# Performance work log

Hardware: AMD Instinct MI355X
Metric: run time of the kernel (lower is better)

Reference implementation:

```python
import jax, jax.numpy as jnp
import numpy as np
from jax import lax

DN = ('NCHW', 'OIHW', 'NCHW')
BN_EPS = 1e-5


def _conv(x, w, pad):
    # pad: list of (lo, hi) for H, W
    return lax.conv_general_dilated(x, w, (1, 1), pad, dimension_numbers=DN)


def _grid_sample_bilinear(img, grid):
    """F.grid_sample(img, grid, align_corners=True, padding_mode='zeros').
    img: [N,C,H,W], grid: [N,Ho,Wo,2] with (x,y) in [-1,1]."""
    N, C, H, W = img.shape
    gx, gy = grid[..., 0], grid[..., 1]
    # align_corners=True mapping to pixel coords
    ix = (gx + 1.0) * 0.5 * (W - 1)
    iy = (gy + 1.0) * 0.5 * (H - 1)
    x0 = jnp.floor(ix)
    y0 = jnp.floor(iy)
    x1 = x0 + 1.0
    y1 = y0 + 1.0
    # bilinear weights
    wa = (x1 - ix) * (y1 - iy)  # top-left (x0,y0)
    wb = (ix - x0) * (y1 - iy)  # top-right (x1,y0)
    wc = (x1 - ix) * (iy - y0)  # bottom-left (x0,y1)
    wd = (ix - x0) * (iy - y0)  # bottom-right (x1,y1)

    imgc = jnp.transpose(img, (0, 2, 3, 1))  # [N,H,W,C]
    b = jnp.arange(N)[:, None, None]

    def gather(xi, yi):
        valid = (xi >= 0) & (xi <= W - 1) & (yi >= 0) & (yi <= H - 1)
        xc = jnp.clip(xi, 0, W - 1).astype(jnp.int32)
        yc = jnp.clip(yi, 0, H - 1).astype(jnp.int32)
        v = imgc[b, yc, xc]  # [N,Ho,Wo,C]
        return v * valid[..., None].astype(img.dtype)

    out = (gather(x0, y0) * wa[..., None] + gather(x1, y0) * wb[..., None]
           + gather(x0, y1) * wc[..., None] + gather(x1, y1) * wd[..., None])
    return jnp.transpose(out, (0, 3, 1, 2))  # [N,C,Ho,Wo]


def setup_inputs() -> dict:
    key = jax.random.key(0)
    ks = jax.random.split(key, 12)
    N, C1, C2 = 8, 512, 256
    H, W = 64, 64
    x1 = jax.random.normal(ks[0], (N, C1, 2 * H, 2 * W), dtype=jnp.float32)
    x2 = jax.random.normal(ks[1], (N, C2, H, W), dtype=jnp.float32)
    w_change = jax.random.normal(ks[2], (C2, C1, 1, 1), dtype=jnp.float32) * 0.02
    b_change = jax.random.normal(ks[3], (C2,), dtype=jnp.float32) * 0.02
    w_cc1 = jax.random.normal(ks[4], (C2, 2 * C2, 1, 1), dtype=jnp.float32) * 0.02
    bn_gamma = 1.0 + 0.1 * jax.random.normal(ks[5], (C2,), dtype=jnp.float32)
    bn_beta = 0.1 * jax.random.normal(ks[6], (C2,), dtype=jnp.float32)
    bn_mean = 0.1 * jax.random.normal(ks[7], (C2,), dtype=jnp.float32)
    bn_var = jax.random.uniform(ks[8], (C2,), dtype=jnp.float32, minval=0.5, maxval=1.5)
    w_cc2 = jax.random.normal(ks[9], (4, C2, 3, 3), dtype=jnp.float32) * 0.02
    return {"x1": x1, "x2": x2, "w_change": w_change, "b_change": b_change,
            "w_cc1": w_cc1, "bn_gamma": bn_gamma, "bn_beta": bn_beta,
            "bn_mean": bn_mean, "bn_var": bn_var, "w_cc2": w_cc2}


def reference(x1, x2, w_change, b_change, w_cc1, bn_gamma, bn_beta, bn_mean, bn_var, w_cc2):
    # MaxPool2d(2,2)
    x1p = lax.reduce_window(x1, -jnp.inf, lax.max, (1, 1, 2, 2), (1, 1, 2, 2), 'VALID')
    # change: 1x1 conv with bias
    x1c = _conv(x1p, w_change, [(0, 0), (0, 0)]) + b_change[None, :, None, None]
    # concat + concat_conv (1x1 conv -> BN(eval) -> ReLU -> 3x3 conv)
    x = jnp.concatenate([x1c, x2], axis=1)
    x = _conv(x, w_cc1, [(0, 0), (0, 0)])
    inv = lax.rsqrt(bn_var + BN_EPS)
    x = (x - bn_mean[None, :, None, None]) * (inv * bn_gamma)[None, :, None, None] + bn_beta[None, :, None, None]
    x = jax.nn.relu(x)
    flow = _conv(x, w_cc2, [(1, 1), (1, 1)])  # [N,4,H,W]
    flow1 = flow[:, :2]
    flow2 = flow[:, 2:]

    N, _, H, W = x1c.shape
    # base grid: [...,0]=x over width, [...,1]=y over height
    xs = jnp.linspace(-1.0, 1.0, W, dtype=x1c.dtype)
    ys = jnp.linspace(-1.0, 1.0, H, dtype=x1c.dtype)
    base = jnp.stack(jnp.meshgrid(xs, ys, indexing='xy'), axis=-1)  # [H,W,2]
    norm = jnp.array([(W - 1) / 2.0, (H - 1) / 2.0], dtype=x1c.dtype)

    grid1 = base[None] + jnp.transpose(flow1, (0, 2, 3, 1)) / norm
    grid2 = base[None] + jnp.transpose(flow2, (0, 2, 3, 1)) / norm

    u1 = _grid_sample_bilinear(x1c, grid1)
    u2 = _grid_sample_bilinear(x2, grid2)
    return u1 + u2
```

## Files before the change

### kernel.cpp

```cpp
#include <hip/hip_runtime.h>
#include <hip/hip_bf16.h>

#define NB 8
#define C1 512
#define C2 256
#define HWSZ 4096
#define BN_EPS 1e-5f
#define P2 264

typedef __hip_bfloat16 bf16;
typedef __hip_bfloat162 bf162;
typedef __attribute__((ext_vector_type(8))) short short8v;
typedef __attribute__((ext_vector_type(4))) float f32x4;

static __device__ inline float us2f(unsigned short u) {
  union { unsigned u32; float f; } c; c.u32 = ((unsigned)u) << 16; return c.f;
}

static __device__ inline unsigned short f2bf(float f) {
  union { bf16 h; unsigned short u; } c;
  c.h = __float2bfloat16(f);
  return c.u;
}

static __device__ inline uint2 pack4(float a, float b, float c, float d) {
  union { uint2 u; bf162 h[2]; } pk;
  pk.h[0] = __float22bfloat162_rn(make_float2(a, b));
  pk.h[1] = __float22bfloat162_rn(make_float2(c, d));
  return pk.u;
}

#define SWA(m_, c_)  (((((c_) >> 3) ^ (((m_) >> 3) & 3)) << 3) + ((c_) & 7))
#define SWA2(m_, c_) (((((c_) >> 3) ^ (((m_) >> 3) & 7)) << 3) + ((c_) & 7))

#define SBARQ() asm volatile("s_waitcnt lgkmcnt(0)\n\ts_barrier" ::: "memory")
#define SBAR()  asm volatile("s_barrier" ::: "memory")
#define LGKM0() asm volatile("s_waitcnt lgkmcnt(0)" ::: "memory")

__global__ __launch_bounds__(256) void k0_prep(
    const float* __restrict__ wch, const float* __restrict__ wcc1,
    const float* __restrict__ wcc2,
    unsigned short* __restrict__ wchB, unsigned short* __restrict__ wcc1B,
    float* __restrict__ wr, float* __restrict__ flow) {
  const int t = blockIdx.x * 256 + threadIdx.x;
  if (t < 262144) {
    const int which = t >> 17;
    const int r = t & 131071;
    const int i = r & 7;
    const int lane = (r >> 3) & 63;
    const int ntile = (r >> 9) & 15;
    const int kstep = r >> 13;
    const int ci = kstep * 32 + (lane >> 4) * 8 + i;
    const int co = ntile * 16 + (lane & 15);
    const float* s = which ? wcc1 : wch;
    unsigned short* d = which ? wcc1B : wchB;
    d[r] = f2bf(s[co * 512 + ci]);
  } else if (t < 262144 + 9216) {
    const int r = t - 262144;
    const int f = r / 2304;
    const int rr = r % 2304;
    const int ci = rr / 9;
    const int tt = rr % 9;
    wr[ci * 36 + (tt / 3) * 12 + (tt % 3) * 4 + f] = wcc2[r];
  } else if (t < 262144 + 9216 + 131072) {
    flow[t - 262144 - 9216] = 0.f;
  }
}

__global__ __launch_bounds__(1024) void k12_fused(
    const float* __restrict__ x1, const float* __restrict__ x2,
    const unsigned short* __restrict__ wchB, const unsigned short* __restrict__ wcc1B,
    const float* __restrict__ bch,
    const float* __restrict__ gamma, const float* __restrict__ beta,
    const float* __restrict__ mean, const float* __restrict__ var,
    const float* __restrict__ wr,
    unsigned short* __restrict__ x1c_nhwc, unsigned short* __restrict__ x2_nhwc,
    float* __restrict__ flow) {
  __shared__ unsigned short As[64 * 40];
  __shared__ unsigned short As2[64 * P2];
  const int tid = threadIdx.x;
  const int lane = tid & 63;
  const int wv = tid >> 6;
  const int lrow = lane & 15;
  const int lgrp = lane >> 4;

  const int m0g = blockIdx.x * 64;
  const int n = m0g >> 12;
  const int hw0 = m0g & 4095;
  const int h = hw0 >> 6;

  f32x4 acc[4];
#pragma unroll
  for (int mt = 0; mt < 4; ++mt) acc[mt] = (f32x4){0.f, 0.f, 0.f, 0.f};

  const int pmi = tid & 31;
  const int ms = pmi * 2;
  const int chA = tid >> 5;

  const float* x1p = x1 + (size_t)n * C1 * 16384 + (size_t)(2 * h) * 128 + 2 * ms;

  float4 t0, b0;
#define LOADA(K0_) do { \
    const float* p_ = x1p + (size_t)((K0_) + chA) * 16384; \
    t0 = *(const float4*)p_;  b0 = *(const float4*)(p_ + 128); \
  } while (0)
#define POOLA(U0_, U1_) do { \
    U0_ = f2bf(fmaxf(fmaxf(t0.x, t0.y), fmaxf(b0.x, b0.y))); \
    U1_ = f2bf(fmaxf(fmaxf(t0.z, t0.w), fmaxf(b0.z, b0.w))); \
  } while (0)

  unsigned short uA0, uA1;
  LOADA(0);
  POOLA(uA0, uA1);
  LOADA(32);

  for (int ks = 0; ks < 16; ++ks) {
    SBARQ();
    As[ms * 40 + SWA(ms, chA)] = uA0;
    As[(ms + 1) * 40 + SWA(ms + 1, chA)] = uA1;
    LGKM0();
    SBAR();

    if (ks < 15) {
      unsigned short uN0, uN1;
      POOLA(uN0, uN1);
      if (ks < 14) LOADA((ks + 2) * 32);
      uA0 = uN0; uA1 = uN1;
    }

    short8v a[4];
#pragma unroll
    for (int mt = 0; mt < 4; ++mt) {
      const int m = mt * 16 + lrow;
      a[mt] = *(const short8v*)&As[m * 40 + SWA(m, lgrp * 8)];
    }
    const short8v b = *(const short8v*)&wchB[(size_t)((ks * 16 + wv) * 64 + lane) * 8];
#pragma unroll
    for (int mt = 0; mt < 4; ++mt)
      acc[mt] = __builtin_amdgcn_mfma_f32_16x16x32_bf16(a[mt], b, acc[mt], 0, 0, 0);
  }

  const int chB = tid >> 5;
  const int mqB = (tid & 31) * 2;
  float2 cf0 = *(const float2*)&x2[((size_t)(n * C2 + chB)) * HWSZ + hw0 + mqB];
  float2 cf1 = *(const float2*)&x2[((size_t)(n * C2 + 32 + chB)) * HWSZ + hw0 + mqB];

  {
    const int co = wv * 16 + lrow;
    const float bias = bch[co];
#pragma unroll
    for (int mt = 0; mt < 4; ++mt) {
      const f32x4 v = acc[mt];
      const uint2 pk = pack4(v.x + bias, v.y + bias, v.z + bias, v.w + bias);
      const int mb = mt * 16 + lgrp * 4;
      As2[(mb + 0) * P2 + SWA2(mb + 0, co)] = (unsigned short)(pk.x & 0xffffu);
      As2[(mb + 1) * P2 + SWA2(mb + 1, co)] = (unsigned short)(pk.x >> 16);
      As2[(mb + 2) * P2 + SWA2(mb + 2, co)] = (unsigned short)(pk.y & 0xffffu);
      As2[(mb + 3) * P2 + SWA2(mb + 3, co)] = (unsigned short)(pk.y >> 16);
      acc[mt] = (f32x4){0.f, 0.f, 0.f, 0.f};
    }
  }
  LGKM0();
  SBAR();

  {
    const int mm = tid >> 4;
    const int cg = (tid & 15) * 16;
    const size_t ob = ((size_t)(m0g + mm)) * 256 + cg;
#pragma unroll
    for (int k = 0; k < 2; ++k) {
      const uint4 v = *(const uint4*)&As2[mm * P2 + SWA2(mm, cg + k * 8)];
      *(uint4*)&x1c_nhwc[ob + k * 8] = v;
    }
  }

#pragma unroll
  for (int ks = 0; ks < 8; ++ks) {
    short8v a[4];
#pragma unroll
    for (int mt = 0; mt < 4; ++mt) {
      const int m = mt * 16 + lrow;
      a[mt] = *(const short8v*)&As2[m * P2 + SWA2(m, ks * 32 + lgrp * 8)];
    }
    const short8v b = *(const short8v*)&wcc1B[(size_t)((ks * 16 + wv) * 64 + lane) * 8];
#pragma unroll
    for (int mt = 0; mt < 4; ++mt)
      acc[mt] = __builtin_amdgcn_mfma_f32_16x16x32_bf16(a[mt], b, acc[mt], 0, 0, 0);
  }

  for (int ks = 8; ks < 16; ++ks) {
    const unsigned short p0 = f2bf(cf0.x);
    const unsigned short p1 = f2bf(cf0.y);
    cf0 = cf1;
    if (ks < 14) {
      cf1 = *(const float2*)&x2[((size_t)(n * C2 + (ks - 6) * 32 + chB)) * HWSZ + hw0 + mqB];
    }
    SBARQ();
    As[(mqB + 0) * 40 + SWA(mqB + 0, chB)] = p0;
    As[(mqB + 1) * 40 + SWA(mqB + 1, chB)] = p1;
    LGKM0();
    SBAR();

    {
      const int m = tid >> 4;
      const int c2 = (tid & 15) * 2;
      const unsigned v = *(const unsigned*)&As[m * 40 + SWA(m, c2)];
      *(unsigned*)&x2_nhwc[((size_t)(m0g + m)) * 256 + (ks - 8) * 32 + c2] = v;
    }

    short8v a[4];
#pragma unroll
    for (int mt = 0; mt < 4; ++mt) {
      const int m = mt * 16 + lrow;
      a[mt] = *(const short8v*)&As[m * 40 + SWA(m, lgrp * 8)];
    }
    const short8v b = *(const short8v*)&wcc1B[(size_t)((ks * 16 + wv) * 64 + lane) * 8];
#pragma unroll
    for (int mt = 0; mt < 4; ++mt)
      acc[mt] = __builtin_amdgcn_mfma_f32_16x16x32_bf16(a[mt], b, acc[mt], 0, 0, 0);
  }

  SBARQ();
  {
    const int co = wv * 16 + lrow;
    const float sc = gamma[co] * rsqrtf(var[co] + BN_EPS);
    const float sh = beta[co] - mean[co] * sc;
#pragma unroll
    for (int mt = 0; mt < 4; ++mt) {
      const f32x4 vv = acc[mt];
      const uint2 pk = pack4(fmaxf(vv.x * sc + sh, 0.f), fmaxf(vv.y * sc + sh, 0.f),
                             fmaxf(vv.z * sc + sh, 0.f), fmaxf(vv.w * sc + sh, 0.f));
      const int mb = mt * 16 + lgrp * 4;
      As2[(mb + 0) * P2 + SWA2(mb + 0, co)] = (unsigned short)(pk.x & 0xffffu);
      As2[(mb + 1) * P2 + SWA2(mb + 1, co)] = (unsigned short)(pk.x >> 16);
      As2[(mb + 2) * P2 + SWA2(mb + 2, co)] = (unsigned short)(pk.y & 0xffffu);
      As2[(mb + 3) * P2 + SWA2(mb + 3, co)] = (unsigned short)(pk.y >> 16);
    }
  }
  LGKM0();
  SBAR();

  {
    const int xp = tid & 63;
    const int fh = tid >> 6;
    const int f = fh & 3;
    const int quarter = fh >> 2;
    float pm = 0.f, pz = 0.f, pp = 0.f;
    for (int ci = quarter * 64; ci < quarter * 64 + 64; ci += 2) {
      const float* w0 = wr + ci * 36 + f;
#pragma unroll
      for (int dx = 0; dx < 3; ++dx) {
        const int xs = xp + dx - 1;
        if ((unsigned)xs >= 64u) continue;
        const unsigned vv = *(const unsigned*)&As2[xs * P2 + SWA2(xs, ci)];
        const float v0 = us2f((unsigned short)(vv & 0xffffu));
        const float v1 = us2f((unsigned short)(vv >> 16));
        const float* wa = w0 + dx * 4;
        const float* wb = wa + 36;
        pm = fmaf(v0, wa[24], fmaf(v1, wb[24], pm));
        pz = fmaf(v0, wa[12], fmaf(v1, wb[12], pz));
        pp = fmaf(v0, wa[0],  fmaf(v1, wb[0],  pp));
      }
    }
    float* fb = flow + ((size_t)(n * 4 + f)) * HWSZ + xp;
    if (h >= 1)  atomicAdd(fb + (h - 1) * 64, pm);
    atomicAdd(fb + h * 64, pz);
    if (h <= 62) atomicAdd(fb + (h + 1) * 64, pp);
  }
#undef LOADA
#undef POOLA
}

__global__ __launch_bounds__(1024) void k4_sample(
    const float* __restrict__ flow,
    const unsigned short* __restrict__ x1c_nhwc,
    const unsigned short* __restrict__ x2_nhwc,
    float* __restrict__ out) {
  __shared__ float outT[256][65];
  __shared__ float flr[4][64];
  __shared__ int   toff[8][64];
  __shared__ float twt[8][64];

  const int tid = threadIdx.x;
  const int n = blockIdx.x >> 6;
  const int h = blockIdx.x & 63;
  const int wl = tid & 63;
  const int q = tid >> 6;

  if (tid < 256) {
    flr[tid >> 6][tid & 63] =
        flow[((size_t)(n * 4 + (tid >> 6))) * HWSZ + h * 64 + (tid & 63)];
  }
  __syncthreads();

  if (tid < 64) {
    const float fxv[2] = {flr[0][tid], flr[2][tid]};
    const float fyv[2] = {flr[1][tid], flr[3][tid]};
#pragma unroll
    for (int s = 0; s < 2; ++s) {
      const float ix = (float)tid + fxv[s], iy = (float)h + fyv[s];
      const float x0f = floorf(ix), y0f = floorf(iy);
      const float fx = ix - x0f, fy = iy - y0f;
      const int x0 = (int)x0f, y0 = (int)y0f, x1i = x0 + 1, y1i = y0 + 1;
      const float vx0 = (x0 >= 0 && x0 < 64) ? 1.f : 0.f;
      const float vx1 = (x1i >= 0 && x1i < 64) ? 1.f : 0.f;
      const float vy0 = (y0 >= 0 && y0 < 64) ? 1.f : 0.f;
      const float vy1 = (y1i >= 0 && y1i < 64) ? 1.f : 0.f;
      const int cx0 = min(max(x0, 0), 63), cx1 = min(max(x1i, 0), 63);
      const int cy0 = min(max(y0, 0), 63), cy1 = min(max(y1i, 0), 63);
      toff[s * 4 + 0][tid] = cy0 * 64 + cx0;
      toff[s * 4 + 1][tid] = cy0 * 64 + cx1;
      toff[s * 4 + 2][tid] = cy1 * 64 + cx0;
      toff[s * 4 + 3][tid] = cy1 * 64 + cx1;
      twt[s * 4 + 0][tid] = (1.f - fx) * (1.f - fy) * vx0 * vy0;
      twt[s * 4 + 1][tid] = fx * (1.f - fy) * vx1 * vy0;
      twt[s * 4 + 2][tid] = (1.f - fx) * fy * vx0 * vy1;
      twt[s * 4 + 3][tid] = fx * fy * vx1 * vy1;
    }
  }
  __syncthreads();

  {
    const unsigned short* pb1 = x1c_nhwc + (size_t)n * HWSZ * 256 + wl * 4;
    const unsigned short* pb2 = x2_nhwc + (size_t)n * HWSZ * 256 + wl * 4;
#pragma unroll
    for (int pp = 0; pp < 4; ++pp) {
      const int p = q * 4 + pp;
      float u0 = 0.f, u1 = 0.f, u2 = 0.f, u3 = 0.f;
#pragma unroll
      for (int t = 0; t < 8; ++t) {
        const int off = toff[t][p];
        const float wt = twt[t][p];
        const unsigned short* rp = (t < 4 ? pb1 : pb2) + (size_t)off * 256;
        const uint2 v = *(const uint2*)rp;
        u0 = fmaf(wt, us2f((unsigned short)(v.x & 0xffffu)), u0);
        u1 = fmaf(wt, us2f((unsigned short)(v.x >> 16)), u1);
        u2 = fmaf(wt, us2f((unsigned short)(v.y & 0xffffu)), u2);
        u3 = fmaf(wt, us2f((unsigned short)(v.y >> 16)), u3);
      }
      outT[wl * 4 + 0][p] = u0;
      outT[wl * 4 + 1][p] = u1;
      outT[wl * 4 + 2][p] = u2;
      outT[wl * 4 + 3][p] = u3;
    }
  }
  __syncthreads();

  {
    const int p = tid & 63;
    const int cg = (tid >> 6) * 16;
    const size_t ob = ((size_t)(n * C2 + cg)) * HWSZ + h * 64 + p;
#pragma unroll
    for (int j = 0; j < 16; ++j) {
      out[ob + (size_t)j * HWSZ] = outT[cg + j][p];
    }
  }
}

extern "C" void kernel_launch(void* const* d_in, const int* in_sizes, int n_in,
                              void* d_out, int out_size, void* d_ws, size_t ws_size,
                              hipStream_t stream) {
  const float* x1      = (const float*)d_in[0];
  const float* x2      = (const float*)d_in[1];
  const float* w_change= (const float*)d_in[2];
  const float* b_change= (const float*)d_in[3];
  const float* w_cc1   = (const float*)d_in[4];
  const float* bn_gamma= (const float*)d_in[5];
  const float* bn_beta = (const float*)d_in[6];
  const float* bn_mean = (const float*)d_in[7];
  const float* bn_var  = (const float*)d_in[8];
  const float* w_cc2   = (const float*)d_in[9];
  float* out = (float*)d_out;

  unsigned short* x1c_nhwc = (unsigned short*)d_ws;
  unsigned short* x2_nhwc  = (unsigned short*)((char*)d_ws + (16u << 20));
  float*          flow     = (float*)((char*)d_ws + (32u << 20));
  unsigned short* wchB     = (unsigned short*)((char*)d_ws + (32u << 20) + (512u << 10));
  unsigned short* wcc1B    = (unsigned short*)((char*)d_ws + (32u << 20) + (768u << 10));
  float*          wr       = (float*)((char*)d_ws + (33u << 20));

  k0_prep<<<1572, 256, 0, stream>>>(w_change, w_cc1, w_cc2, wchB, wcc1B, wr, flow);
  k12_fused<<<512, 1024, 0, stream>>>(x1, x2, wchB, wcc1B, b_change,
                                      bn_gamma, bn_beta, bn_mean, bn_var, wr,
                                      x1c_nhwc, x2_nhwc, flow);
  k4_sample<<<512, 1024, 0, stream>>>(flow, x1c_nhwc, x2_nhwc, out);
}
```

Measured before the change: 135.0 us.

## Register-resident A tiles with 4 waves each computing all output channels

Reorganizes the fused pool+1x1 conv kernel so each of 4 waves holds its 16-row A fragment in registers and accumulates all 256 output channels, removing the per-k LDS staging and block barriers. The pooled x1 and x2 inputs are converted to bf16 straight into MFMA operands with double-buffered global loads. This trades barrier/LDS overhead for higher register use, fewer waves per block, and a longer serial 3x3 conv reduction per thread.

New measurement: 268.5 us. 1.99x slower.

```diff
diff --git a/kernel.cpp b/kernel.cpp
--- a/kernel.cpp
+++ b/kernel.cpp
@@ -23,19 +23,16 @@
   return c.u;
 }
 
-static __device__ inline uint2 pack4(float a, float b, float c, float d) {
-  union { uint2 u; bf162 h[2]; } pk;
-  pk.h[0] = __float22bfloat162_rn(make_float2(a, b));
-  pk.h[1] = __float22bfloat162_rn(make_float2(c, d));
+static __device__ inline unsigned pack2(float a, float b) {
+  union { unsigned u; bf162 h; } pk;
+  pk.h = __float22bfloat162_rn(make_float2(a, b));
   return pk.u;
 }
 
-#define SWA(m_, c_)  (((((c_) >> 3) ^ (((m_) >> 3) & 3)) << 3) + ((c_) & 7))
 #define SWA2(m_, c_) (((((c_) >> 3) ^ (((m_) >> 3) & 7)) << 3) + ((c_) & 7))
 
-#define SBARQ() asm volatile("s_waitcnt lgkmcnt(0)\n\ts_barrier" ::: "memory")
+#define LGKM0() asm volatile("s_waitcnt lgkmcnt(0)" ::: "memory")
 #define SBAR()  asm volatile("s_barrier" ::: "memory")
-#define LGKM0() asm volatile("s_waitcnt lgkmcnt(0)" ::: "memory")
 
 __global__ __launch_bounds__(256) void k0_prep(
     const float* __restrict__ wch, const float* __restrict__ wcc1,
@@ -67,7 +64,7 @@
   }
 }
 
-__global__ __launch_bounds__(1024) void k12_fused(
+__global__ __launch_bounds__(256) void k12_fused(
     const float* __restrict__ x1, const float* __restrict__ x2,
     const unsigned short* __restrict__ wchB, const unsigned short* __restrict__ wcc1B,
     const float* __restrict__ bch,
@@ -76,11 +73,10 @@
     const float* __restrict__ wr,
     unsigned short* __restrict__ x1c_nhwc, unsigned short* __restrict__ x2_nhwc,
     float* __restrict__ flow) {
-  __shared__ unsigned short As[64 * 40];
   __shared__ unsigned short As2[64 * P2];
   const int tid = threadIdx.x;
   const int lane = tid & 63;
-  const int wv = tid >> 6;
+  const int wq = tid >> 6;
   const int lrow = lane & 15;
   const int lgrp = lane >> 4;
 
@@ -88,165 +84,152 @@
   const int n = m0g >> 12;
   const int hw0 = m0g & 4095;
   const int h = hw0 >> 6;
-
-  f32x4 acc[4];
-#pragma unroll
-  for (int mt = 0; mt < 4; ++mt) acc[mt] = (f32x4){0.f, 0.f, 0.f, 0.f};
-
-  const int pmi = tid & 31;
-  const int ms = pmi * 2;
-  const int chA = tid >> 5;
-
-  const float* x1p = x1 + (size_t)n * C1 * 16384 + (size_t)(2 * h) * 128 + 2 * ms;
-
-  float4 t0, b0;
-#define LOADA(K0_) do { \
-    const float* p_ = x1p + (size_t)((K0_) + chA) * 16384; \
-    t0 = *(const float4*)p_;  b0 = *(const float4*)(p_ + 128); \
-  } while (0)
-#define POOLA(U0_, U1_) do { \
-    U0_ = f2bf(fmaxf(fmaxf(t0.x, t0.y), fmaxf(b0.x, b0.y))); \
-    U1_ = f2bf(fmaxf(fmaxf(t0.z, t0.w), fmaxf(b0.z, b0.w))); \
-  } while (0)
-
-  unsigned short uA0, uA1;
-  LOADA(0);
-  POOLA(uA0, uA1);
-  LOADA(32);
-
-  for (int ks = 0; ks < 16; ++ks) {
-    SBARQ();
-    As[ms * 40 + SWA(ms, chA)] = uA0;
-    As[(ms + 1) * 40 + SWA(ms + 1, chA)] = uA1;
-    LGKM0();
-    SBAR();
-
-    if (ks < 15) {
-      unsigned short uN0, uN1;
-      POOLA(uN0, uN1);
-      if (ks < 14) LOADA((ks + 2) * 32);
-      uA0 = uN0; uA1 = uN1;
-    }
-
-    short8v a[4];
-#pragma unroll
-    for (int mt = 0; mt < 4; ++mt) {
-      const int m = mt * 16 + lrow;
-      a[mt] = *(const short8v*)&As[m * 40 + SWA(m, lgrp * 8)];
-    }
-    const short8v b = *(const short8v*)&wchB[(size_t)((ks * 16 + wv) * 64 + lane) * 8];
-#pragma unroll
-    for (int mt = 0; mt < 4; ++mt)
-      acc[mt] = __builtin_amdgcn_mfma_f32_16x16x32_bf16(a[mt], b, acc[mt], 0, 0, 0);
-  }
-
-  const int chB = tid >> 5;
-  const int mqB = (tid & 31) * 2;
-  float2 cf0 = *(const float2*)&x2[((size_t)(n * C2 + chB)) * HWSZ + hw0 + mqB];
-  float2 cf1 = *(const float2*)&x2[((size_t)(n * C2 + 32 + chB)) * HWSZ + hw0 + mqB];
-
-  {
-    const int co = wv * 16 + lrow;
+  const int rowA = wq * 16 + lrow;
+
+  f32x4 acc[16];
+#pragma unroll
+  for (int nt = 0; nt < 16; ++nt) acc[nt] = (f32x4){0.f, 0.f, 0.f, 0.f};
+
+  const float* x1b = x1 + (size_t)n * C1 * 16384 + (size_t)(2 * h) * 128 + 2 * rowA;
+
+  float2 tA[8], bA[8], tB[8], bB[8];
+#define LOADX(KS_, T_, B_) do { \
+    const float* pp_ = x1b + (size_t)((KS_) * 32 + lgrp * 8) * 16384; \
+    _Pragma("unroll") \
+    for (int i_ = 0; i_ < 8; ++i_) { \
+      T_[i_] = *(const float2*)(pp_ + (size_t)i_ * 16384); \
+      B_[i_] = *(const float2*)(pp_ + (size_t)i_ * 16384 + 128); \
+    } \
+  } while (0)
+#define PKA(T_, B_, AV_) do { \
+    union { unsigned uu[4]; short8v s; } c_; \
+    _Pragma("unroll") \
+    for (int i2_ = 0; i2_ < 4; ++i2_) { \
+      const float v0_ = fmaxf(fmaxf(T_[2 * i2_].x, T_[2 * i2_].y), \
+                              fmaxf(B_[2 * i2_].x, B_[2 * i2_].y)); \
+      const float v1_ = fmaxf(fmaxf(T_[2 * i2_ + 1].x, T_[2 * i2_ + 1].y), \
+                              fmaxf(B_[2 * i2_ + 1].x, B_[2 * i2_ + 1].y)); \
+      c_.uu[i2_] = pack2(v0_, v1_); \
+    } \
+    AV_ = c_.s; \
+  } while (0)
+#define MFMAW(KS_, A_, WP_) do { \
+    _Pragma("unroll") \
+    for (int nt_ = 0; nt_ < 16; ++nt_) { \
+      const short8v b_ = *(const short8v*)&WP_[(size_t)(((KS_) * 16 + nt_) * 64 + lane) * 8]; \
+      acc[nt_] = __builtin_amdgcn_mfma_f32_16x16x32_bf16(A_, b_, acc[nt_], 0, 0, 0); \
+    } \
+  } while (0)
+
+  LOADX(0, tA, bA);
+  LOADX(1, tB, bB);
+  for (int ks2 = 0; ks2 < 8; ++ks2) {
+    const int ks = ks2 * 2;
+    short8v a0;
+    PKA(tA, bA, a0);
+    if (ks2 < 7) LOADX(ks + 2, tA, bA);
+    MFMAW(ks, a0, wchB);
+    short8v a1;
+    PKA(tB, bB, a1);
+    if (ks2 < 7) LOADX(ks + 3, tB, bB);
+    MFMAW(ks + 1, a1, wchB);
+  }
+
+#pragma unroll
+  for (int nt = 0; nt < 16; ++nt) {
+    const int co = nt * 16 + lrow;
     const float bias = bch[co];
-#pragma unroll
-    for (int mt = 0; mt < 4; ++mt) {
-      const f32x4 v = acc[mt];
-      const uint2 pk = pack4(v.x + bias, v.y + bias, v.z + bias, v.w + bias);
-      const int mb = mt * 16 + lgrp * 4;
-      As2[(mb + 0) * P2 + SWA2(mb + 0, co)] = (unsigned short)(pk.x & 0xffffu);
-      As2[(mb + 1) * P2 + SWA2(mb + 1, co)] = (unsigned short)(pk.x >> 16);
-      As2[(mb + 2) * P2 + SWA2(mb + 2, co)] = (unsigned short)(pk.y & 0xffffu);
-      As2[(mb + 3) * P2 + SWA2(mb + 3, co)] = (unsigned short)(pk.y >> 16);
-      acc[mt] = (f32x4){0.f, 0.f, 0.f, 0.f};
+    const f32x4 v = acc[nt];
+    const float vv[4] = {v.x + bias, v.y + bias, v.z + bias, v.w + bias};
+#pragma unroll
+    for (int j = 0; j < 4; ++j) {
+      const int r = wq * 16 + lgrp * 4 + j;
+      As2[r * P2 + SWA2(r, co)] = f2bf(vv[j]);
+    }
+    acc[nt] = (f32x4){0.f, 0.f, 0.f, 0.f};
+  }
+
+  {
+    const int er = wq * 16 + (lane >> 2);
+    const int ec = (lane & 3) * 64;
+    const size_t ob = ((size_t)(m0g + er)) * 256 + ec;
+#pragma unroll
+    for (int k = 0; k < 8; ++k) {
+      const uint4 v = *(const uint4*)&As2[er * P2 + SWA2(er, ec + k * 8)];
+      *(uint4*)&x1c_nhwc[ob + k * 8] = v;
+    }
+  }
+
+#pragma unroll
+  for (int ks = 0; ks < 8; ++ks) {
+    const short8v a = *(const short8v*)&As2[rowA * P2 + SWA2(rowA, ks * 32 + lgrp * 8)];
+    MFMAW(ks, a, wcc1B);
+  }
+
+  float x2v0[8], x2v1[8];
+#define LOADX2(KS_, V_) do { \
+    const float* p2_ = x2 + ((size_t)(n * C2 + ((KS_) - 8) * 32 + lgrp * 8)) * HWSZ + hw0 + rowA; \
+    _Pragma("unroll") \
+    for (int i_ = 0; i_ < 8; ++i_) V_[i_] = p2_[(size_t)i_ * HWSZ]; \
+  } while (0)
+#define PROC2(KS_, V_) do { \
+    union { unsigned short us[8]; short8v s; } c_; \
+    _Pragma("unroll") \
+    for (int i_ = 0; i_ < 8; ++i_) c_.us[i_] = f2bf(V_[i_]); \
+    const int sb_ = rowA * P2 + SWA2(rowA, ((KS_) - 8) * 32 + lgrp * 8); \
+    _Pragma("unroll") \
+    for (int i_ = 0; i_ < 8; ++i_) As2[sb_ + i_] = c_.us[i_]; \
+    MFMAW(KS_, c_.s, wcc1B); \
+  } while (0)
+
+  LOADX2(8, x2v0);
+  LOADX2(9, x2v1);
+  for (int ks2 = 0; ks2 < 4; ++ks2) {
+    const int ks = 8 + ks2 * 2;
+    if (ks2 < 3) {
+      PROC2(ks, x2v0);
+      LOADX2(ks + 2, x2v0);
+      PROC2(ks + 1, x2v1);
+      LOADX2(ks + 3, x2v1);
+    } else {
+      PROC2(ks, x2v0);
+      PROC2(ks + 1, x2v1);
+    }
+  }
+
+  {
+    const int er = wq * 16 + (lane >> 2);
+    const int ec = (lane & 3) * 64;
+    const size_t ob = ((size_t)(m0g + er)) * 256 + ec;
+#pragma unroll
+    for (int k = 0; k < 8; ++k) {
+      const uint4 v = *(const uint4*)&As2[er * P2 + SWA2(er, ec + k * 8)];
+      *(uint4*)&x2_nhwc[ob + k * 8] = v;
+    }
+  }
+
+#pragma unroll
+  for (int nt = 0; nt < 16; ++nt) {
+    const int co = nt * 16 + lrow;
+    const float sc = gamma[co] * rsqrtf(var[co] + BN_EPS);
+    const float sh = beta[co] - mean[co] * sc;
+    const f32x4 v = acc[nt];
+    const float vv[4] = {fmaxf(v.x * sc + sh, 0.f), fmaxf(v.y * sc + sh, 0.f),
+                         fmaxf(v.z * sc + sh, 0.f), fmaxf(v.w * sc + sh, 0.f)};
+#pragma unroll
+    for (int j = 0; j < 4; ++j) {
+      const int r = wq * 16 + lgrp * 4 + j;
+      As2[r * P2 + SWA2(r, co)] = f2bf(vv[j]);
     }
   }
   LGKM0();
   SBAR();
 
   {
-    const int mm = tid >> 4;
-    const int cg = (tid & 15) * 16;
-    const size_t ob = ((size_t)(m0g + mm)) * 256 + cg;
-#pragma unroll
-    for (int k = 0; k < 2; ++k) {
-      const uint4 v = *(const uint4*)&As2[mm * P2 + SWA2(mm, cg + k * 8)];
-      *(uint4*)&x1c_nhwc[ob + k * 8] = v;
-    }
-  }
-
-#pragma unroll
-  for (int ks = 0; ks < 8; ++ks) {
-    short8v a[4];
-#pragma unroll
-    for (int mt = 0; mt < 4; ++mt) {
-      const int m = mt * 16 + lrow;
-      a[mt] = *(const short8v*)&As2[m * P2 + SWA2(m, ks * 32 + lgrp * 8)];
-    }
-    const short8v b = *(const short8v*)&wcc1B[(size_t)((ks * 16 + wv) * 64 + lane) * 8];
-#pragma unroll
-    for (int mt = 0; mt < 4; ++mt)
-      acc[mt] = __builtin_amdgcn_mfma_f32_16x16x32_bf16(a[mt], b, acc[mt], 0, 0, 0);
-  }
-
-  for (int ks = 8; ks < 16; ++ks) {
-    const unsigned short p0 = f2bf(cf0.x);
-    const unsigned short p1 = f2bf(cf0.y);
-    cf0 = cf1;
-    if (ks < 14) {
-      cf1 = *(const float2*)&x2[((size_t)(n * C2 + (ks - 6) * 32 + chB)) * HWSZ + hw0 + mqB];
-    }
-    SBARQ();
-    As[(mqB + 0) * 40 + SWA(mqB + 0, chB)] = p0;
-    As[(mqB + 1) * 40 + SWA(mqB + 1, chB)] = p1;
-    LGKM0();
-    SBAR();
-
-    {
-      const int m = tid >> 4;
-      const int c2 = (tid & 15) * 2;
-      const unsigned v = *(const unsigned*)&As[m * 40 + SWA(m, c2)];
-      *(unsigned*)&x2_nhwc[((size_t)(m0g + m)) * 256 + (ks - 8) * 32 + c2] = v;
-    }
-
-    short8v a[4];
-#pragma unroll
-    for (int mt = 0; mt < 4; ++mt) {
-      const int m = mt * 16 + lrow;
-      a[mt] = *(const short8v*)&As[m * 40 + SWA(m, lgrp * 8)];
-    }
-    const short8v b = *(const short8v*)&wcc1B[(size_t)((ks * 16 + wv) * 64 + lane) * 8];
-#pragma unroll
-    for (int mt = 0; mt < 4; ++mt)
-      acc[mt] = __builtin_amdgcn_mfma_f32_16x16x32_bf16(a[mt], b, acc[mt], 0, 0, 0);
-  }
-
-  SBARQ();
-  {
-    const int co = wv * 16 + lrow;
-    const float sc = gamma[co] * rsqrtf(var[co] + BN_EPS);
-    const float sh = beta[co] - mean[co] * sc;
-#pragma unroll
-    for (int mt = 0; mt < 4; ++mt) {
-      const f32x4 vv = acc[mt];
-      const uint2 pk = pack4(fmaxf(vv.x * sc + sh, 0.f), fmaxf(vv.y * sc + sh, 0.f),
-                             fmaxf(vv.z * sc + sh, 0.f), fmaxf(vv.w * sc + sh, 0.f));
-      const int mb = mt * 16 + lgrp * 4;
-      As2[(mb + 0) * P2 + SWA2(mb + 0, co)] = (unsigned short)(pk.x & 0xffffu);
-      As2[(mb + 1) * P2 + SWA2(mb + 1, co)] = (unsigned short)(pk.x >> 16);
-      As2[(mb + 2) * P2 + SWA2(mb + 2, co)] = (unsigned short)(pk.y & 0xffffu);
-      As2[(mb + 3) * P2 + SWA2(mb + 3, co)] = (unsigned short)(pk.y >> 16);
-    }
-  }
-  LGKM0();
-  SBAR();
-
-  {
     const int xp = tid & 63;
-    const int fh = tid >> 6;
-    const int f = fh & 3;
-    const int quarter = fh >> 2;
+    const int f = tid >> 6;
     float pm = 0.f, pz = 0.f, pp = 0.f;
-    for (int ci = quarter * 64; ci < quarter * 64 + 64; ci += 2) {
+    for (int ci = 0; ci < 256; ci += 2) {
       const float* w0 = wr + ci * 36 + f;
 #pragma unroll
       for (int dx = 0; dx < 3; ++dx) {
@@ -267,8 +250,11 @@
     atomicAdd(fb + h * 64, pz);
     if (h <= 62) atomicAdd(fb + (h + 1) * 64, pp);
   }
-#undef LOADA
-#undef POOLA
+#undef LOADX
+#undef PKA
+#undef MFMAW
+#undef LOADX2
+#undef PROC2
 }
 
 __global__ __launch_bounds__(1024) void k4_sample(
@@ -380,8 +366,8 @@
   float*          wr       = (float*)((char*)d_ws + (33u << 20));
 
   k0_prep<<<1572, 256, 0, stream>>>(w_change, w_cc1, w_cc2, wchB, wcc1B, wr, flow);
-  k12_fused<<<512, 1024, 0, stream>>>(x1, x2, wchB, wcc1B, b_change,
-                                      bn_gamma, bn_beta, bn_mean, bn_var, wr,
-                                      x1c_nhwc, x2_nhwc, flow);
+  k12_fused<<<512, 256, 0, stream>>>(x1, x2, wchB, wcc1B, b_change,
+                                     bn_gamma, bn_beta, bn_mean, bn_var, wr,
+                                     x1c_nhwc, x2_nhwc, flow);
   k4_sample<<<512, 1024, 0, stream>>>(flow, x1c_nhwc, x2_nhwc, out);
 }
```
